# Kernel tuning notes

Measured on AMD Instinct MI355X. Metric: run time of the kernel, lower is better.

## Reference

```python
import jax, jax.numpy as jnp
import numpy as np

NEG_SLOPE = 0.01  # torch leaky_relu default

N_NODES = 100000
N_EDGES = 1600000
D = 64
N_BBOX = 4096


def setup_inputs() -> dict:
    key = jax.random.key(0)
    ks = jax.random.split(key, 9)
    x = jax.random.normal(ks[0], (N_NODES, D), dtype=jnp.float32)
    edge_index = jax.random.randint(ks[1], (2, N_EDGES), 0, N_NODES, dtype=jnp.int64)
    bbox = jax.random.randint(ks[2], (N_BBOX,), 0, N_NODES, dtype=jnp.int64)
    s = 1.0 / np.sqrt(D)
    W1_rel = jax.random.normal(ks[3], (D, D), dtype=jnp.float32) * s
    b1 = jax.random.normal(ks[4], (D,), dtype=jnp.float32) * s
    W1_root = jax.random.normal(ks[5], (D, D), dtype=jnp.float32) * s
    W2_rel = jax.random.normal(ks[6], (D, D), dtype=jnp.float32) * s
    b2 = jax.random.normal(ks[7], (D,), dtype=jnp.float32) * s
    W2_root = jax.random.normal(ks[8], (D, D), dtype=jnp.float32) * s
    return {"x": x, "edge_index": edge_index, "bbox": bbox,
            "W1_rel": W1_rel, "b1": b1, "W1_root": W1_root,
            "W2_rel": W2_rel, "b2": b2, "W2_root": W2_root}


def graph_conv(x, src, dst, W_rel, b, W_root):
    # PyG GraphConv: out_i = W_rel @ (sum_{j in N(i)} x_j) + b + W_root @ x_i
    msg = x[src]                                        # [E, D] gather
    agg = jax.ops.segment_sum(msg, dst, num_segments=x.shape[0])  # [N, D] scatter-add
    return agg @ W_rel + b + x @ W_root


def reference(x, edge_index, bbox, W1_rel, b1, W1_root, W2_rel, b2, W2_root):
    src, dst = edge_index[0], edge_index[1]
    h = graph_conv(x, src, dst, W1_rel, b1, W1_root)
    h = jax.nn.leaky_relu(h, NEG_SLOPE)
    # dropout is identity at inference (training=False)
    h = graph_conv(h, src, dst, W2_rel, b2, W2_root)
    h = jax.nn.leaky_relu(h, NEG_SLOPE)
    return h[bbox]
```

## Files before the change

kernel.cpp:

```cpp
#include <hip/hip_runtime.h>

#define N_NODES 100000
#define N_EDGES 1600000
#define D 64
#define N_BBOX 4096
#define CAP 64

__device__ __forceinline__ float readlane_f(float v, int l) {
  return __int_as_float(__builtin_amdgcn_readlane(__float_as_int(v), l));
}
__device__ __forceinline__ int bperm(int srclane, int v) {
  return __builtin_amdgcn_ds_bpermute(srclane << 2, v);
}
__device__ __forceinline__ float lrelu(float v) {
  return fmaxf(v, 0.01f * v);
}

__global__ __launch_bounds__(256) void mark_kernel(const int* __restrict__ bbox,
                                                   int* __restrict__ is_bbox,
                                                   int* __restrict__ needed) {
  int t = blockIdx.x * blockDim.x + threadIdx.x;
  if (t < N_BBOX) {
    int n = bbox[t];
    is_bbox[n] = 1;
    needed[n] = 1;
  }
}

__global__ __launch_bounds__(256) void mark_needed_kernel(
    const int* __restrict__ src, const int* __restrict__ dst,
    const int* __restrict__ is_bbox, int* __restrict__ needed) {
  int e = blockIdx.x * blockDim.x + threadIdx.x;
  if (e >= N_EDGES) return;
  int d = dst[e];
  if (is_bbox[d]) needed[src[e]] = 1;
}

__global__ __launch_bounds__(256) void fill_kernel(const int* __restrict__ src,
                                                   const int* __restrict__ dst,
                                                   const int* __restrict__ needed,
                                                   int* __restrict__ cnt,
                                                   int* __restrict__ slots) {
  int e = blockIdx.x * blockDim.x + threadIdx.x;
  if (e >= N_EDGES) return;
  int d = dst[e];
  if (!needed[d]) return;
  int p = atomicAdd(&cnt[d], 1);
  if (p < CAP) slots[(size_t)d * CAP + p] = src[e];
}

__global__ __launch_bounds__(256) void gather1_kernel(const float4* __restrict__ x4,
                                                      const int* __restrict__ needed,
                                                      const int* __restrict__ cnt,
                                                      const int* __restrict__ slots,
                                                      float4* __restrict__ agg4) {
  const int wid = (blockIdx.x * blockDim.x + threadIdx.x) >> 6;
  if (wid >= N_NODES) return;
  if (!needed[wid]) return;
  const int lane = threadIdx.x & 63;
  const int g = lane >> 4, c = lane & 15;

  int n = cnt[wid];
  n = (n > CAP) ? CAP : n;
  const int myslot = (lane < n) ? slots[(size_t)wid * CAP + lane] : 0;

  float4 acc = make_float4(0.f, 0.f, 0.f, 0.f);
  for (int e0 = 0; e0 < n; e0 += 32) {
    int idx[8], s[8];
    float4 v[8];
#pragma unroll
    for (int u = 0; u < 8; u++) {
      idx[u] = e0 + u * 4 + g;
      s[u] = bperm(idx[u], myslot);
    }
#pragma unroll
    for (int u = 0; u < 8; u++) {
      v[u] = make_float4(0.f, 0.f, 0.f, 0.f);
      if (idx[u] < n) v[u] = x4[(size_t)s[u] * 16 + c];
    }
#pragma unroll
    for (int u = 0; u < 8; u++) {
      acc.x += v[u].x; acc.y += v[u].y; acc.z += v[u].z; acc.w += v[u].w;
    }
  }
  acc.x += __shfl_xor(acc.x, 16); acc.y += __shfl_xor(acc.y, 16);
  acc.z += __shfl_xor(acc.z, 16); acc.w += __shfl_xor(acc.w, 16);
  acc.x += __shfl_xor(acc.x, 32); acc.y += __shfl_xor(acc.y, 32);
  acc.z += __shfl_xor(acc.z, 32); acc.w += __shfl_xor(acc.w, 32);
  if (g == 0) agg4[(size_t)wid * 16 + c] = acc;
}

__global__ __launch_bounds__(256, 1) void dense1_kernel(
    const float* __restrict__ x, const int* __restrict__ needed,
    const float* __restrict__ W1rel, const float* __restrict__ b1,
    const float* __restrict__ W1root, float* __restrict__ hbuf) {
  const int lane = threadIdx.x & 63;
  const int wid = (blockIdx.x * blockDim.x + threadIdx.x) >> 6;
  const int nw = (gridDim.x * blockDim.x) >> 6;

  float wrel[D], wroot[D];
#pragma unroll
  for (int k = 0; k < D; k++) {
    wrel[k] = W1rel[k * D + lane];
    wroot[k] = W1root[k * D + lane];
  }
  const float bj = b1[lane];

  for (int i = wid; i < N_NODES; i += nw) {
    if (!needed[i]) continue;
    const float a = hbuf[(size_t)i * D + lane];
    const float xi = x[(size_t)i * D + lane];
    float s0 = 0.f, s1 = 0.f, s2 = 0.f, s3 = 0.f;
#pragma unroll
    for (int k = 0; k < D; k += 2) {
      s0 += readlane_f(a, k) * wrel[k];
      s1 += readlane_f(xi, k) * wroot[k];
      s2 += readlane_f(a, k + 1) * wrel[k + 1];
      s3 += readlane_f(xi, k + 1) * wroot[k + 1];
    }
    hbuf[(size_t)i * D + lane] = lrelu(bj + ((s0 + s1) + (s2 + s3)));
  }
}

__global__ __launch_bounds__(256, 1) void layer2_kernel(
    const float4* __restrict__ h4, const int* __restrict__ cnt,
    const int* __restrict__ slots, const int* __restrict__ bbox,
    const float* __restrict__ W2rel, const float* __restrict__ b2,
    const float* __restrict__ W2root, float* __restrict__ out) {
  const int t = (blockIdx.x * blockDim.x + threadIdx.x) >> 6;
  if (t >= N_BBOX) return;
  const int lane = threadIdx.x & 63;
  const int g = lane >> 4, c = lane & 15;

  float wrel[D], wroot[D];
#pragma unroll
  for (int k = 0; k < D; k++) {
    wrel[k] = W2rel[k * D + lane];
    wroot[k] = W2root[k * D + lane];
  }
  const float bj = b2[lane];

  const int node = __builtin_amdgcn_readfirstlane(bbox[t]);
  int n = cnt[node];
  n = (n > CAP) ? CAP : n;
  const int myslot = (lane < n) ? slots[(size_t)node * CAP + lane] : 0;

  float4 acc = make_float4(0.f, 0.f, 0.f, 0.f);
  for (int e0 = 0; e0 < n; e0 += 32) {
    int idx[8], s[8];
    float4 v[8];
#pragma unroll
    for (int u = 0; u < 8; u++) {
      idx[u] = e0 + u * 4 + g;
      s[u] = bperm(idx[u], myslot);
    }
#pragma unroll
    for (int u = 0; u < 8; u++) {
      v[u] = make_float4(0.f, 0.f, 0.f, 0.f);
      if (idx[u] < n) v[u] = h4[(size_t)s[u] * 16 + c];
    }
#pragma unroll
    for (int u = 0; u < 8; u++) {
      acc.x += v[u].x; acc.y += v[u].y; acc.z += v[u].z; acc.w += v[u].w;
    }
  }
  acc.x += __shfl_xor(acc.x, 16); acc.y += __shfl_xor(acc.y, 16);
  acc.z += __shfl_xor(acc.z, 16); acc.w += __shfl_xor(acc.w, 16);
  acc.x += __shfl_xor(acc.x, 32); acc.y += __shfl_xor(acc.y, 32);
  acc.z += __shfl_xor(acc.z, 32); acc.w += __shfl_xor(acc.w, 32);

  const float hi = ((const float*)h4)[(size_t)node * D + lane];
  float s0 = 0.f, s1 = 0.f, s2 = 0.f, s3 = 0.f;
#pragma unroll
  for (int k = 0; k < D; k += 2) {
    const float a0 = (k & 2) ? readlane_f(acc.z, k >> 2) : readlane_f(acc.x, k >> 2);
    const float a1 = ((k + 1) & 2) ? readlane_f(acc.w, (k + 1) >> 2)
                                   : readlane_f(acc.y, (k + 1) >> 2);
    s0 += a0 * wrel[k];
    s1 += readlane_f(hi, k) * wroot[k];
    s2 += a1 * wrel[k + 1];
    s3 += readlane_f(hi, k + 1) * wroot[k + 1];
  }
  out[(size_t)t * D + lane] = lrelu(bj + ((s0 + s1) + (s2 + s3)));
}


extern "C" void kernel_launch(void* const* d_in, const int* in_sizes, int n_in,
                              void* d_out, int out_size, void* d_ws, size_t ws_size,
                              hipStream_t stream) {
  const float* x = (const float*)d_in[0];
  const int* ei = (const int*)d_in[1];
  const int* src = ei;
  const int* dst = ei + N_EDGES;
  const int* bbox = (const int*)d_in[2];
  const float* W1rel = (const float*)d_in[3];
  const float* b1 = (const float*)d_in[4];
  const float* W1root = (const float*)d_in[5];
  const float* W2rel = (const float*)d_in[6];
  const float* b2 = (const float*)d_in[7];
  const float* W2root = (const float*)d_in[8];
  float* out = (float*)d_out;

  char* ws = (char*)d_ws;
  size_t off = 0;
  auto alloc = [&](size_t bytes) -> char* {
    char* p = ws + off;
    off = (off + bytes + 511) & ~(size_t)511;
    return p;
  };
  int* is_bbox = (int*)alloc(N_NODES * sizeof(int));
  int* needed = (int*)alloc(N_NODES * sizeof(int));
  int* cnt = (int*)alloc(N_NODES * sizeof(int));
  char* zero_end = ws + off;
  int* slots = (int*)alloc((size_t)N_NODES * CAP * sizeof(int));
  float* hbuf = (float*)alloc((size_t)N_NODES * D * sizeof(float));

  hipMemsetAsync(is_bbox, 0, (size_t)(zero_end - (char*)is_bbox), stream);
  mark_kernel<<<(N_BBOX + 255) / 256, 256, 0, stream>>>(bbox, is_bbox, needed);
  mark_needed_kernel<<<(N_EDGES + 255) / 256, 256, 0, stream>>>(src, dst, is_bbox,
                                                                needed);
  fill_kernel<<<(N_EDGES + 255) / 256, 256, 0, stream>>>(src, dst, needed, cnt,
                                                         slots);
  gather1_kernel<<<(N_NODES + 3) / 4, 256, 0, stream>>>(
      (const float4*)x, needed, cnt, slots, (float4*)hbuf);
  dense1_kernel<<<2048, 256, 0, stream>>>(x, needed, W1rel, b1, W1root, hbuf);
  layer2_kernel<<<(N_BBOX + 3) / 4, 256, 0, stream>>>(
      (const float4*)hbuf, cnt, slots, bbox, W2rel, b2, W2root, out);
}
```

Before: 214.0 us.

## Fuse layer-1 gather into dense kernel and use bitmasks for needed flags

Merges the layer-1 neighbor gather into the dense matmul kernel, so the aggregated features stay in registers instead of going to hbuf and being read back. The is_bbox and needed flag arrays become packed bitmaps set with atomicOr, which shrinks the memset and the flag lookups. The fused kernel runs a persistent grid with 256-register weight arrays, so the gather has lower occupancy and less memory-level parallelism (unroll reduced from 8 to 4). The bitmap writes also add atomic contention.

```diff
diff --git a/kernel.cpp b/kernel.cpp
--- a/kernel.cpp
+++ b/kernel.cpp
@@ -5,6 +5,7 @@
 #define D 64
 #define N_BBOX 4096
 #define CAP 64
+#define NBITW 3136
 
 __device__ __forceinline__ float readlane_f(float v, int l) {
   return __int_as_float(__builtin_amdgcn_readlane(__float_as_int(v), l));
@@ -15,88 +16,56 @@
 __device__ __forceinline__ float lrelu(float v) {
   return fmaxf(v, 0.01f * v);
 }
+__device__ __forceinline__ bool testbit(const unsigned* bits, int i) {
+  return (bits[i >> 5] >> (i & 31)) & 1u;
+}
 
 __global__ __launch_bounds__(256) void mark_kernel(const int* __restrict__ bbox,
-                                                   int* __restrict__ is_bbox,
-                                                   int* __restrict__ needed) {
+                                                   unsigned* __restrict__ is_bbox_bits,
+                                                   unsigned* __restrict__ needed_bits) {
   int t = blockIdx.x * blockDim.x + threadIdx.x;
   if (t < N_BBOX) {
     int n = bbox[t];
-    is_bbox[n] = 1;
-    needed[n] = 1;
+    unsigned m = 1u << (n & 31);
+    atomicOr(&is_bbox_bits[n >> 5], m);
+    atomicOr(&needed_bits[n >> 5], m);
   }
 }
 
 __global__ __launch_bounds__(256) void mark_needed_kernel(
     const int* __restrict__ src, const int* __restrict__ dst,
-    const int* __restrict__ is_bbox, int* __restrict__ needed) {
+    const unsigned* __restrict__ is_bbox_bits, unsigned* __restrict__ needed_bits) {
   int e = blockIdx.x * blockDim.x + threadIdx.x;
   if (e >= N_EDGES) return;
   int d = dst[e];
-  if (is_bbox[d]) needed[src[e]] = 1;
+  if (testbit(is_bbox_bits, d)) {
+    int s = src[e];
+    atomicOr(&needed_bits[s >> 5], 1u << (s & 31));
+  }
 }
 
 __global__ __launch_bounds__(256) void fill_kernel(const int* __restrict__ src,
                                                    const int* __restrict__ dst,
-                                                   const int* __restrict__ needed,
+                                                   const unsigned* __restrict__ needed_bits,
                                                    int* __restrict__ cnt,
                                                    int* __restrict__ slots) {
   int e = blockIdx.x * blockDim.x + threadIdx.x;
   if (e >= N_EDGES) return;
   int d = dst[e];
-  if (!needed[d]) return;
+  if (!testbit(needed_bits, d)) return;
   int p = atomicAdd(&cnt[d], 1);
   if (p < CAP) slots[(size_t)d * CAP + p] = src[e];
 }
 
-__global__ __launch_bounds__(256) void gather1_kernel(const float4* __restrict__ x4,
-                                                      const int* __restrict__ needed,
-                                                      const int* __restrict__ cnt,
-                                                      const int* __restrict__ slots,
-                                                      float4* __restrict__ agg4) {
-  const int wid = (blockIdx.x * blockDim.x + threadIdx.x) >> 6;
-  if (wid >= N_NODES) return;
-  if (!needed[wid]) return;
-  const int lane = threadIdx.x & 63;
-  const int g = lane >> 4, c = lane & 15;
-
-  int n = cnt[wid];
-  n = (n > CAP) ? CAP : n;
-  const int myslot = (lane < n) ? slots[(size_t)wid * CAP + lane] : 0;
-
-  float4 acc = make_float4(0.f, 0.f, 0.f, 0.f);
-  for (int e0 = 0; e0 < n; e0 += 32) {
-    int idx[8], s[8];
-    float4 v[8];
-#pragma unroll
-    for (int u = 0; u < 8; u++) {
-      idx[u] = e0 + u * 4 + g;
-      s[u] = bperm(idx[u], myslot);
-    }
-#pragma unroll
-    for (int u = 0; u < 8; u++) {
-      v[u] = make_float4(0.f, 0.f, 0.f, 0.f);
-      if (idx[u] < n) v[u] = x4[(size_t)s[u] * 16 + c];
-    }
-#pragma unroll
-    for (int u = 0; u < 8; u++) {
-      acc.x += v[u].x; acc.y += v[u].y; acc.z += v[u].z; acc.w += v[u].w;
-    }
-  }
-  acc.x += __shfl_xor(acc.x, 16); acc.y += __shfl_xor(acc.y, 16);
-  acc.z += __shfl_xor(acc.z, 16); acc.w += __shfl_xor(acc.w, 16);
-  acc.x += __shfl_xor(acc.x, 32); acc.y += __shfl_xor(acc.y, 32);
-  acc.z += __shfl_xor(acc.z, 32); acc.w += __shfl_xor(acc.w, 32);
-  if (g == 0) agg4[(size_t)wid * 16 + c] = acc;
-}
-
-__global__ __launch_bounds__(256, 1) void dense1_kernel(
-    const float* __restrict__ x, const int* __restrict__ needed,
+__global__ __launch_bounds__(256, 1) void layer1_fused_kernel(
+    const float4* __restrict__ x4, const unsigned* __restrict__ needed_bits,
+    const int* __restrict__ cnt, const int* __restrict__ slots,
     const float* __restrict__ W1rel, const float* __restrict__ b1,
     const float* __restrict__ W1root, float* __restrict__ hbuf) {
   const int lane = threadIdx.x & 63;
-  const int wid = (blockIdx.x * blockDim.x + threadIdx.x) >> 6;
+  const int wid0 = (blockIdx.x * blockDim.x + threadIdx.x) >> 6;
   const int nw = (gridDim.x * blockDim.x) >> 6;
+  const int g = lane >> 4, c = lane & 15;
 
   float wrel[D], wroot[D];
 #pragma unroll
@@ -106,16 +75,46 @@
   }
   const float bj = b1[lane];
 
-  for (int i = wid; i < N_NODES; i += nw) {
-    if (!needed[i]) continue;
-    const float a = hbuf[(size_t)i * D + lane];
-    const float xi = x[(size_t)i * D + lane];
+  for (int i = wid0; i < N_NODES; i += nw) {
+    if (!testbit(needed_bits, i)) continue;
+    int n = cnt[i];
+    n = (n > CAP) ? CAP : n;
+    const int myslot = (lane < n) ? slots[(size_t)i * CAP + lane] : 0;
+
+    float4 acc = make_float4(0.f, 0.f, 0.f, 0.f);
+    for (int e0 = 0; e0 < n; e0 += 16) {
+      int idx[4], s[4];
+      float4 v[4];
+#pragma unroll
+      for (int u = 0; u < 4; u++) {
+        idx[u] = e0 + u * 4 + g;
+        s[u] = bperm(idx[u], myslot);
+      }
+#pragma unroll
+      for (int u = 0; u < 4; u++) {
+        v[u] = make_float4(0.f, 0.f, 0.f, 0.f);
+        if (idx[u] < n) v[u] = x4[(size_t)s[u] * 16 + c];
+      }
+#pragma unroll
+      for (int u = 0; u < 4; u++) {
+        acc.x += v[u].x; acc.y += v[u].y; acc.z += v[u].z; acc.w += v[u].w;
+      }
+    }
+    acc.x += __shfl_xor(acc.x, 16); acc.y += __shfl_xor(acc.y, 16);
+    acc.z += __shfl_xor(acc.z, 16); acc.w += __shfl_xor(acc.w, 16);
+    acc.x += __shfl_xor(acc.x, 32); acc.y += __shfl_xor(acc.y, 32);
+    acc.z += __shfl_xor(acc.z, 32); acc.w += __shfl_xor(acc.w, 32);
+
+    const float xi = ((const float*)x4)[(size_t)i * D + lane];
     float s0 = 0.f, s1 = 0.f, s2 = 0.f, s3 = 0.f;
 #pragma unroll
     for (int k = 0; k < D; k += 2) {
-      s0 += readlane_f(a, k) * wrel[k];
+      const float a0 = (k & 2) ? readlane_f(acc.z, k >> 2) : readlane_f(acc.x, k >> 2);
+      const float a1 = ((k + 1) & 2) ? readlane_f(acc.w, (k + 1) >> 2)
+                                     : readlane_f(acc.y, (k + 1) >> 2);
+      s0 += a0 * wrel[k];
       s1 += readlane_f(xi, k) * wroot[k];
-      s2 += readlane_f(a, k + 1) * wrel[k + 1];
+      s2 += a1 * wrel[k + 1];
       s3 += readlane_f(xi, k + 1) * wroot[k + 1];
     }
     hbuf[(size_t)i * D + lane] = lrelu(bj + ((s0 + s1) + (s2 + s3)));
@@ -208,22 +207,22 @@
     off = (off + bytes + 511) & ~(size_t)511;
     return p;
   };
-  int* is_bbox = (int*)alloc(N_NODES * sizeof(int));
-  int* needed = (int*)alloc(N_NODES * sizeof(int));
+  unsigned* is_bbox_bits = (unsigned*)alloc(NBITW * sizeof(unsigned));
+  unsigned* needed_bits = (unsigned*)alloc(NBITW * sizeof(unsigned));
   int* cnt = (int*)alloc(N_NODES * sizeof(int));
   char* zero_end = ws + off;
   int* slots = (int*)alloc((size_t)N_NODES * CAP * sizeof(int));
   float* hbuf = (float*)alloc((size_t)N_NODES * D * sizeof(float));
 
-  hipMemsetAsync(is_bbox, 0, (size_t)(zero_end - (char*)is_bbox), stream);
-  mark_kernel<<<(N_BBOX + 255) / 256, 256, 0, stream>>>(bbox, is_bbox, needed);
-  mark_needed_kernel<<<(N_EDGES + 255) / 256, 256, 0, stream>>>(src, dst, is_bbox,
-                                                                needed);
-  fill_kernel<<<(N_EDGES + 255) / 256, 256, 0, stream>>>(src, dst, needed, cnt,
-                                                         slots);
-  gather1_kernel<<<(N_NODES + 3) / 4, 256, 0, stream>>>(
-      (const float4*)x, needed, cnt, slots, (float4*)hbuf);
-  dense1_kernel<<<2048, 256, 0, stream>>>(x, needed, W1rel, b1, W1root, hbuf);
+  hipMemsetAsync(is_bbox_bits, 0, (size_t)(zero_end - (char*)is_bbox_bits), stream);
+  mark_kernel<<<(N_BBOX + 255) / 256, 256, 0, stream>>>(bbox, is_bbox_bits,
+                                                        needed_bits);
+  mark_needed_kernel<<<(N_EDGES + 255) / 256, 256, 0, stream>>>(
+      src, dst, is_bbox_bits, needed_bits);
+  fill_kernel<<<(N_EDGES + 255) / 256, 256, 0, stream>>>(src, dst, needed_bits,
+                                                         cnt, slots);
+  layer1_fused_kernel<<<2048, 256, 0, stream>>>(
+      (const float4*)x, needed_bits, cnt, slots, W1rel, b1, W1root, hbuf);
   layer2_kernel<<<(N_BBOX + 3) / 4, 256, 0, stream>>>(
       (const float4*)hbuf, cnt, slots, bbox, W2rel, b2, W2root, out);
 }
```

New measurement: 226.4 us. 5.8% more time.
